# Kernel tuning notes

Measured on AMD Instinct MI355X. Metric: run time of the kernel, lower is better.

## Reference

```python
import jax, jax.numpy as jnp
import numpy as np

N_NODES = 50000


def setup_inputs() -> dict:
    key = jax.random.key(0)
    k = jax.random.split(key, 5)
    x = jax.random.normal(k[0], (N_NODES, 64), dtype=jnp.float32)
    edge_index = jax.random.randint(k[1], (2, 800000), 0, N_NODES, dtype=jnp.int64)
    # Glorot-ish init for weights
    W1 = jax.random.normal(k[2], (64, 64), dtype=jnp.float32) * (1.0 / np.sqrt(64))
    b1 = jnp.zeros((64,), dtype=jnp.float32)
    W2 = jax.random.normal(k[3], (64, 16), dtype=jnp.float32) * (1.0 / np.sqrt(64))
    b2 = jnp.zeros((16,), dtype=jnp.float32)
    return {"x": x, "edge_index": edge_index, "W1": W1, "b1": b1, "W2": W2, "b2": b2}


def _gcn_conv(h, row, col, W, b, n_nodes):
    # PyG GCNConv: add self-loops, symmetric deg normalization, linear, scatter-add.
    h = h @ W                                   # [N, out]
    deg = jax.ops.segment_sum(jnp.ones_like(col, dtype=h.dtype), col,
                              num_segments=n_nodes)          # in-degree incl. self-loops
    dinv = jnp.where(deg > 0, jax.lax.rsqrt(deg), 0.0)       # deg^{-1/2}
    norm = dinv[row] * dinv[col]                             # [E]
    msg = h[row] * norm[:, None]                             # gather + scale, [E, out]
    out = jax.ops.segment_sum(msg, col, num_segments=n_nodes)  # scatter-add at targets
    return out + b


def reference(x, edge_index, W1, b1, W2, b2):
    n = x.shape[0]
    loops = jnp.arange(n, dtype=edge_index.dtype)
    row = jnp.concatenate([edge_index[0], loops])  # sources (with self-loops)
    col = jnp.concatenate([edge_index[1], loops])  # targets (with self-loops)
    h = _gcn_conv(x, row, col, W1, b1, n)
    h = jax.nn.relu(h)
    h = _gcn_conv(h, row, col, W2, b2, n)
    return jax.nn.log_softmax(h, axis=1)
```

## Files before the change

### kernel.cpp

```cpp
#include <hip/hip_runtime.h>
#include <hip/hip_bf16.h>
#include <math.h>


#define BLK 256
#define EPB 2048
#define GSH 9
#define GMASK 511
#define GMAX 128
#define QCAP 10240

typedef __attribute__((ext_vector_type(8))) short short8;
typedef __attribute__((ext_vector_type(4))) float float4v;
typedef __attribute__((ext_vector_type(4))) unsigned short ushort4v;

__device__ __forceinline__ short f2bf(float f) {
    __hip_bfloat16 h = __float2bfloat16(f);
    union { __hip_bfloat16 h; short s; } u; u.h = h; return u.s;
}
__device__ __forceinline__ float bf2f(short s) {
    union { short s; __hip_bfloat16 h; } u; u.s = s; return __bfloat162float(u.h);
}
__device__ __forceinline__ float ldf(const void* p, long long i, int f32) {
    if (f32) return ((const float*)p)[i];
    return __bfloat162float(((const __hip_bfloat16*)p)[i]);
}
__device__ __forceinline__ float4v mfma_bf16(short8 a, short8 b, float4v c) {
    return __builtin_amdgcn_mfma_f32_16x16x32_bf16(a, b, c, 0, 0, 0);
}

__global__ void init_k(const void* edge_raw, const unsigned short* xraw, long long n_nodes,
                       const void* W1, const void* W2, const void* b1, const void* b2,
                       int* flags, short* wT1, short* wT2, float* b1f, float* b2f,
                       int* gtail, int G) {
    __shared__ int bad, cnt;
    int tid = threadIdx.x;
    if (tid == 0) { bad = 0; cnt = 0; }
    __syncthreads();
    const long long* p = (const long long*)edge_raw;
    for (int i = tid; i < 1024; i += BLK) {
        long long v = p[i];
        if (v < 0 || v >= n_nodes) bad = 1;
    }
    int e = (xraw[2 * tid] >> 7) & 0xFF;
    int inr = (e >= 96 && e <= 130) ? 1 : 0;
    __syncthreads();
    if (inr) atomicAdd(&cnt, 1);
    __syncthreads();
    int f32 = (cnt < 128) ? 1 : 0;
    if (tid == 0) { flags[0] = bad ? 0 : 1; flags[1] = f32; }
    for (int i = tid; i < G * 16; i += BLK) gtail[i] = 0;
    for (int idx = tid; idx < 4096; idx += BLK) {
        int k = idx >> 6, j = idx & 63;
        wT1[j * 64 + k] = f2bf(ldf(W1, idx, f32));
    }
    for (int idx = tid; idx < 1024; idx += BLK) {
        int k = idx >> 4, j = idx & 15;
        wT2[j * 64 + k] = f2bf(ldf(W2, idx, f32));
    }
    if (tid < 64) b1f[tid] = ldf(b1, tid, f32);
    if (tid < 16) b2f[tid] = ldf(b2, tid, f32);
}

__global__ __launch_bounds__(BLK) void binAmm1_k(const void* edge_raw, const void* x,
                                                 const int* __restrict__ flags, int E,
                                                 int* gtail, int* __restrict__ queue,
                                                 const short* __restrict__ wT1,
                                                 unsigned short* __restrict__ h1,
                                                 int N, int G, int nblkA) {
    int bid = blockIdx.x, tid = threadIdx.x;
    if (bid < nblkA) {
        __shared__ int hist[GMAX], base[GMAX];
        for (int g = tid; g < G; g += BLK) hist[g] = 0;
        __syncthreads();
        int is64 = flags[0];
        int e0 = bid * EPB;
        int r[8], c[8], pos[8];
        const long long* p64 = (const long long*)edge_raw;
        const int* p32 = (const int*)edge_raw;
        #pragma unroll
        for (int i = 0; i < 8; ++i) {
            int e = e0 + i * BLK + tid;
            int rr = -1, cc = 0;
            if (e < E) {
                if (is64) { rr = (int)p64[e]; cc = (int)p64[(long long)E + e]; }
                else      { rr = p32[e];      cc = p32[E + e]; }
            }
            r[i] = rr; c[i] = cc;
            pos[i] = (rr >= 0) ? atomicAdd(&hist[cc >> GSH], 1) : 0;
        }
        __syncthreads();
        for (int g = tid; g < G; g += BLK) {
            int h = hist[g];
            base[g] = h ? atomicAdd(&gtail[g << 4], h) : 0;
        }
        __syncthreads();
        #pragma unroll
        for (int i = 0; i < 8; ++i) {
            if (r[i] >= 0) {
                int g = c[i] >> GSH;
                int idx = base[g] + pos[i];
                if (idx < QCAP)
                    queue[(long long)g * QCAP + idx] = (r[i] << GSH) | (c[i] & GMASK);
            }
        }
    } else {
        int wave = ((bid - nblkA) << 2) + (tid >> 6);
        int lane = tid & 63;
        int node0 = wave << 4;
        if (node0 >= N) return;
        int m = lane & 15, quad = lane >> 4;
        int node = node0 + m;
        int nc = node < N ? node : N - 1;
        short8 a0, a1;
        if (flags[1]) {
            const float* xf = (const float*)x + ((long long)nc << 6) + quad * 8;
            #pragma unroll
            for (int i = 0; i < 8; ++i) { a0[i] = f2bf(xf[i]); a1[i] = f2bf(xf[32 + i]); }
        } else {
            const unsigned short* xb = (const unsigned short*)x + ((long long)nc << 6) + quad * 8;
            a0 = *(const short8*)xb;
            a1 = *(const short8*)(xb + 32);
        }
        const short8* wp = (const short8*)wT1;
        #pragma unroll
        for (int jt = 0; jt < 4; ++jt) {
            float4v cc = {0.f, 0.f, 0.f, 0.f};
            cc = mfma_bf16(a0, wp[((jt * 16 + m) << 3) + quad], cc);
            cc = mfma_bf16(a1, wp[((jt * 16 + m) << 3) + 4 + quad], cc);
            #pragma unroll
            for (int r2 = 0; r2 < 4; ++r2) {
                int n2 = node0 + (quad << 2) + r2;
                if (n2 < N) h1[((long long)n2 << 6) + jt * 16 + m] = (unsigned short)f2bf(cc[r2]);
            }
        }
    }
}

__global__ __launch_bounds__(1024) void binB_k(const int* __restrict__ gtail,
                                               const int* __restrict__ queue,
                                               unsigned short* __restrict__ srcs,
                                               int* __restrict__ cntf,
                                               float* __restrict__ dinv, int N) {
    __shared__ int lcnt[512];
    int g = blockIdx.x, tid = threadIdx.x;
    for (int i = tid; i < 512; i += 1024) lcnt[i] = 0;
    __syncthreads();
    int len = gtail[g << 4];
    if (len > QCAP) len = QCAP;
    const int* q = queue + (long long)g * QCAP;
    int n0 = g << GSH;
    for (int i = tid; i < len; i += 1024) {
        int u = q[i];
        int cl = u & GMASK, rr = u >> GSH;
        int pos = atomicAdd(&lcnt[cl], 1);
        if (pos < 64) srcs[((long long)(n0 + cl) << 6) + pos] = (unsigned short)rr;
    }
    __syncthreads();
    for (int i = tid; i < 512; i += 1024) {
        int gn = n0 + i;
        if (gn < N) {
            cntf[gn] = lcnt[i];
            dinv[gn] = rsqrtf((float)lcnt[i] + 1.0f);
        }
    }
}

__global__ __launch_bounds__(BLK) void agg1mm2_k(const unsigned short* __restrict__ h1,
                                                 const int* __restrict__ cntf,
                                                 const float* __restrict__ dinv,
                                                 const unsigned short* __restrict__ srcs,
                                                 const short* __restrict__ wT2,
                                                 const float* __restrict__ b1f,
                                                 unsigned short* __restrict__ h2, int N) {
    __shared__ short a_lds[16][72];
    int b = blockIdx.x, tid = threadIdx.x;
    int wv = tid >> 6, lane = tid & 63;
    int seg = lane & 7;
    int es  = lane >> 3;
    #pragma unroll
    for (int k = 0; k < 4; ++k) {
        int nl = wv * 4 + k;
        int gn = (b << 4) + nl;
        int gnc = gn < N ? gn : N - 1;
        float acc[8];
        #pragma unroll
        for (int i = 0; i < 8; ++i) acc[i] = 0.f;
        float dc = 1.f;
        if (gn < N) {
            int dg = cntf[gn];
            int m = dg < 64 ? dg : 64;
            const unsigned short* sp = srcs + ((long long)gn << 6);
            dc = dinv[gn];
            for (int e = es; e < m; e += 8) {
                int r = sp[e];
                float d = dinv[r];
                short8 v = *(const short8*)(h1 + ((long long)r << 6) + (seg << 3));
                #pragma unroll
                for (int i = 0; i < 8; ++i) acc[i] += bf2f(v[i]) * d;
            }
        }
        #pragma unroll
        for (int i = 0; i < 8; ++i) {
            acc[i] += __shfl_xor(acc[i], 8, 64);
            acc[i] += __shfl_xor(acc[i], 16, 64);
            acc[i] += __shfl_xor(acc[i], 32, 64);
        }
        if (es == 0) {
            short8 vs = *(const short8*)(h1 + ((long long)gnc << 6) + (seg << 3));
            short8 o;
            #pragma unroll
            for (int i = 0; i < 8; ++i) {
                float hg = (gn < N) ? (acc[i] + bf2f(vs[i]) * dc) * dc : 0.f;
                o[i] = f2bf(fmaxf(hg + b1f[(seg << 3) + i], 0.f));
            }
            *(short8*)&a_lds[nl][seg << 3] = o;
        }
    }
    __syncthreads();
    if (wv == 0) {
        int m = lane & 15, quad = lane >> 4;
        short8 a0 = *(const short8*)&a_lds[m][quad * 8];
        short8 a1 = *(const short8*)&a_lds[m][quad * 8 + 32];
        const short8* wp = (const short8*)wT2;
        float4v c = {0.f, 0.f, 0.f, 0.f};
        c = mfma_bf16(a0, wp[(m << 3) + quad], c);
        c = mfma_bf16(a1, wp[(m << 3) + 4 + quad], c);
        #pragma unroll
        for (int r = 0; r < 4; ++r) {
            int n2 = (b << 4) + (quad << 2) + r;
            if (n2 < N) h2[((long long)n2 << 4) + m] = (unsigned short)f2bf(c[r] * dinv[n2]);
        }
    }
}

__global__ __launch_bounds__(BLK) void agg2sm_k(const unsigned short* __restrict__ h2,
                                                const int* __restrict__ cntf,
                                                const unsigned short* __restrict__ srcs,
                                                const float* __restrict__ b2f,
                                                const int* __restrict__ flags,
                                                void* __restrict__ out, int N) {
    int c = (blockIdx.x * BLK + threadIdx.x) >> 6;
    if (c >= N) return;
    int lane = threadIdx.x & 63;
    int seg = lane & 1;
    int es  = lane >> 1;
    int dg = cntf[c];
    int m = dg < 64 ? dg : 64;
    const unsigned short* sp = srcs + ((long long)c << 6);
    float acc[8];
    #pragma unroll
    for (int i = 0; i < 8; ++i) acc[i] = 0.f;
    for (int e = es; e < m; e += 32) {
        int r = sp[e];
        short8 v = *(const short8*)(h2 + ((long long)r << 4) + (seg << 3));
        #pragma unroll
        for (int i = 0; i < 8; ++i) acc[i] += bf2f(v[i]);
    }
    #pragma unroll
    for (int i = 0; i < 8; ++i) {
        acc[i] += __shfl_xor(acc[i], 2, 64);
        acc[i] += __shfl_xor(acc[i], 4, 64);
        acc[i] += __shfl_xor(acc[i], 8, 64);
        acc[i] += __shfl_xor(acc[i], 16, 64);
        acc[i] += __shfl_xor(acc[i], 32, 64);
    }
    float dc = rsqrtf((float)dg + 1.0f);
    short8 vs = *(const short8*)(h2 + ((long long)c << 4) + (seg << 3));
    float logit[8];
    float mx = -1e30f;
    #pragma unroll
    for (int i = 0; i < 8; ++i) {
        logit[i] = (acc[i] + bf2f(vs[i])) * dc + b2f[(seg << 3) + i];
        mx = fmaxf(mx, logit[i]);
    }
    mx = fmaxf(mx, __shfl_xor(mx, 1, 64));
    float s = 0.f;
    #pragma unroll
    for (int i = 0; i < 8; ++i) s += expf(logit[i] - mx);
    s += __shfl_xor(s, 1, 64);
    float lse = mx + logf(s);
    if (es == 0) {
        if (flags[1]) {
            float* op = (float*)out + ((long long)c << 4) + (seg << 3);
            #pragma unroll
            for (int i = 0; i < 8; ++i) op[i] = logit[i] - lse;
        } else {
            __hip_bfloat16* op = (__hip_bfloat16*)out + ((long long)c << 4) + (seg << 3);
            #pragma unroll
            for (int i = 0; i < 8; ++i) op[i] = __float2bfloat16(logit[i] - lse);
        }
    }
}

extern "C" void kernel_launch(void* const* d_in, const int* in_sizes, int n_in,
                              void* d_out, int out_size, void* d_ws, size_t ws_size,
                              hipStream_t stream) {
    const void* x        = d_in[0];
    const void* edge_raw = d_in[1];
    const void* W1       = d_in[2];
    const void* b1       = d_in[3];
    const void* W2       = d_in[4];
    const void* b2       = d_in[5];

    const int N = in_sizes[0] / 64;
    const int E = in_sizes[1] / 2;
    const int G = (N + 511) >> 9;
    const int NBUCK = (N + 15) / 16;

    char* ws = (char*)d_ws;
    size_t o = 0;
    auto take = [&](size_t bytes) { char* p = ws + o; o += (bytes + 255) & ~(size_t)255; return p; };
    int*            flags  = (int*)take(256);
    int*            gtail  = (int*)take((size_t)G * 64);
    int*            queue  = (int*)take((size_t)G * QCAP * 4);
    unsigned short* srcs   = (unsigned short*)take((size_t)N * 64 * 2);
    int*            cntf   = (int*)take((size_t)N * 4);
    float*          dinv   = (float*)take((size_t)N * 4);
    float*          b1f    = (float*)take(64 * 4);
    float*          b2f    = (float*)take(16 * 4);
    short*          wT1    = (short*)take(4096 * 2);
    short*          wT2    = (short*)take(1024 * 2);
    unsigned short* h1     = (unsigned short*)take((size_t)N * 64 * 2);
    unsigned short* h2     = (unsigned short*)take((size_t)N * 16 * 2);

    int nblkA = (E + EPB - 1) / EPB;
    int nblkW = ((N + 15) / 16 + 3) / 4;
    int nblkG = ((size_t)N * 64 + BLK - 1) / BLK;

    init_k<<<1, BLK, 0, stream>>>(edge_raw, (const unsigned short*)x, (long long)N,
                                  W1, W2, b1, b2, flags, wT1, wT2, b1f, b2f, gtail, G);
    binAmm1_k<<<nblkA + nblkW, BLK, 0, stream>>>(edge_raw, x, flags, E, gtail, queue,
                                                 wT1, h1, N, G, nblkA);
    binB_k<<<G, 1024, 0, stream>>>(gtail, queue, srcs, cntf, dinv, N);
    agg1mm2_k<<<NBUCK, BLK, 0, stream>>>(h1, cntf, dinv, srcs, wT2, b1f, h2, N);
    agg2sm_k<<<nblkG, BLK, 0, stream>>>(h2, cntf, srcs, b2f, flags, d_out, N);
}
```

Measured before the change: 161.7 us.

## Aggregate directly from bucketed edge queues with LDS float atomics, drop CSR build

Buckets shrink to 128 target nodes. The per-node source list (srcs/cntf) is no longer built; a lightweight degree kernel counts in-degrees from the queue. Both aggregation kernels now run one block per bucket, stream that bucket's edge queue and scatter-add gathered features into a shared-memory accumulator with LDS atomics, then apply normalization, MM2 and log-softmax. This removes the 64-neighbor cap and one intermediate write/read pass, at the cost of many LDS float atomics, fewer and larger blocks, and a fixed QCAP of 3072 per bucket that could overflow on skewed graphs.

```diff
diff --git a/kernel.cpp b/kernel.cpp
--- a/kernel.cpp
+++ b/kernel.cpp
@@ -4,15 +4,14 @@
 
 
 #define BLK 256
-#define EPB 2048
-#define GSH 9
-#define GMASK 511
-#define GMAX 128
-#define QCAP 10240
+#define EPB 4096
+#define GSH 7
+#define GMASK 127
+#define GMAX 512
+#define QCAP 3072
 
 typedef __attribute__((ext_vector_type(8))) short short8;
 typedef __attribute__((ext_vector_type(4))) float float4v;
-typedef __attribute__((ext_vector_type(4))) unsigned short ushort4v;
 
 __device__ __forceinline__ short f2bf(float f) {
     __hip_bfloat16 h = __float2bfloat16(f);
@@ -75,11 +74,11 @@
         __syncthreads();
         int is64 = flags[0];
         int e0 = bid * EPB;
-        int r[8], c[8], pos[8];
+        int r[16], c[16], pos[16];
         const long long* p64 = (const long long*)edge_raw;
         const int* p32 = (const int*)edge_raw;
         #pragma unroll
-        for (int i = 0; i < 8; ++i) {
+        for (int i = 0; i < 16; ++i) {
             int e = e0 + i * BLK + tid;
             int rr = -1, cc = 0;
             if (e < E) {
@@ -96,7 +95,7 @@
         }
         __syncthreads();
         #pragma unroll
-        for (int i = 0; i < 8; ++i) {
+        for (int i = 0; i < 16; ++i) {
             if (r[i] >= 0) {
                 int g = c[i] >> GSH;
                 int idx = base[g] + pos[i];
@@ -137,158 +136,143 @@
     }
 }
 
-__global__ __launch_bounds__(1024) void binB_k(const int* __restrict__ gtail,
-                                               const int* __restrict__ queue,
-                                               unsigned short* __restrict__ srcs,
-                                               int* __restrict__ cntf,
-                                               float* __restrict__ dinv, int N) {
-    __shared__ int lcnt[512];
+__global__ __launch_bounds__(BLK) void deg_k(const int* __restrict__ gtail,
+                                             const int* __restrict__ queue,
+                                             float* __restrict__ dinv, int N) {
+    __shared__ int cnt[128];
     int g = blockIdx.x, tid = threadIdx.x;
-    for (int i = tid; i < 512; i += 1024) lcnt[i] = 0;
+    if (tid < 128) cnt[tid] = 0;
     __syncthreads();
     int len = gtail[g << 4];
     if (len > QCAP) len = QCAP;
     const int* q = queue + (long long)g * QCAP;
-    int n0 = g << GSH;
-    for (int i = tid; i < len; i += 1024) {
-        int u = q[i];
-        int cl = u & GMASK, rr = u >> GSH;
-        int pos = atomicAdd(&lcnt[cl], 1);
-        if (pos < 64) srcs[((long long)(n0 + cl) << 6) + pos] = (unsigned short)rr;
-    }
-    __syncthreads();
-    for (int i = tid; i < 512; i += 1024) {
-        int gn = n0 + i;
-        if (gn < N) {
-            cntf[gn] = lcnt[i];
-            dinv[gn] = rsqrtf((float)lcnt[i] + 1.0f);
-        }
-    }
-}
-
-__global__ __launch_bounds__(BLK) void agg1mm2_k(const unsigned short* __restrict__ h1,
-                                                 const int* __restrict__ cntf,
+    for (int i = tid; i < len; i += BLK)
+        atomicAdd(&cnt[q[i] & GMASK], 1);
+    __syncthreads();
+    if (tid < 128) {
+        int gn = (g << GSH) + tid;
+        if (gn < N) dinv[gn] = rsqrtf((float)cnt[tid] + 1.0f);
+    }
+}
+
+__global__ __launch_bounds__(512) void agg1mm2_k(const unsigned short* __restrict__ h1,
                                                  const float* __restrict__ dinv,
-                                                 const unsigned short* __restrict__ srcs,
+                                                 const int* __restrict__ gtail,
+                                                 const int* __restrict__ queue,
                                                  const short* __restrict__ wT2,
                                                  const float* __restrict__ b1f,
                                                  unsigned short* __restrict__ h2, int N) {
-    __shared__ short a_lds[16][72];
-    int b = blockIdx.x, tid = threadIdx.x;
+    __shared__ float acc[128][67];
+    int g = blockIdx.x, tid = threadIdx.x;
+    float* af = &acc[0][0];
+    for (int i = tid; i < 128 * 67; i += 512) af[i] = 0.f;
+    __syncthreads();
+    int len = gtail[g << 4];
+    if (len > QCAP) len = QCAP;
+    const int* q = queue + (long long)g * QCAP;
     int wv = tid >> 6, lane = tid & 63;
-    int seg = lane & 7;
-    int es  = lane >> 3;
-    #pragma unroll
-    for (int k = 0; k < 4; ++k) {
-        int nl = wv * 4 + k;
-        int gn = (b << 4) + nl;
-        int gnc = gn < N ? gn : N - 1;
-        float acc[8];
-        #pragma unroll
-        for (int i = 0; i < 8; ++i) acc[i] = 0.f;
-        float dc = 1.f;
-        if (gn < N) {
-            int dg = cntf[gn];
-            int m = dg < 64 ? dg : 64;
-            const unsigned short* sp = srcs + ((long long)gn << 6);
-            dc = dinv[gn];
-            for (int e = es; e < m; e += 8) {
-                int r = sp[e];
-                float d = dinv[r];
-                short8 v = *(const short8*)(h1 + ((long long)r << 6) + (seg << 3));
-                #pragma unroll
-                for (int i = 0; i < 8; ++i) acc[i] += bf2f(v[i]) * d;
-            }
-        }
+    int es = lane >> 3, seg = lane & 7;
+    for (int e0 = wv * 8; e0 < len; e0 += 64) {
+        int e = e0 + es;
+        if (e < len) {
+            int u = q[e];
+            int r = u >> GSH, cl = u & GMASK;
+            float d = dinv[r];
+            short8 v = *(const short8*)(h1 + ((long long)r << 6) + (seg << 3));
+            #pragma unroll
+            for (int i = 0; i < 8; ++i)
+                atomicAdd(&acc[cl][(seg << 3) + i], bf2f(v[i]) * d);
+        }
+    }
+    __syncthreads();
+    {
+        int m = lane & 15, quad = lane >> 4;
+        int node = (wv << 4) + m;
+        int gn = (g << GSH) + node;
+        int gc = gn < N ? gn : N - 1;
+        float dc = dinv[gc];
+        const unsigned short* hs = h1 + ((long long)gc << 6);
+        short8 s0 = *(const short8*)(hs + quad * 8);
+        short8 s1 = *(const short8*)(hs + quad * 8 + 32);
+        short8 a0, a1;
         #pragma unroll
         for (int i = 0; i < 8; ++i) {
-            acc[i] += __shfl_xor(acc[i], 8, 64);
-            acc[i] += __shfl_xor(acc[i], 16, 64);
-            acc[i] += __shfl_xor(acc[i], 32, 64);
-        }
-        if (es == 0) {
-            short8 vs = *(const short8*)(h1 + ((long long)gnc << 6) + (seg << 3));
-            short8 o;
-            #pragma unroll
-            for (int i = 0; i < 8; ++i) {
-                float hg = (gn < N) ? (acc[i] + bf2f(vs[i]) * dc) * dc : 0.f;
-                o[i] = f2bf(fmaxf(hg + b1f[(seg << 3) + i], 0.f));
-            }
-            *(short8*)&a_lds[nl][seg << 3] = o;
-        }
-    }
-    __syncthreads();
-    if (wv == 0) {
-        int m = lane & 15, quad = lane >> 4;
-        short8 a0 = *(const short8*)&a_lds[m][quad * 8];
-        short8 a1 = *(const short8*)&a_lds[m][quad * 8 + 32];
+            int f0 = quad * 8 + i, f1 = f0 + 32;
+            float v0 = (acc[node][f0] + bf2f(s0[i]) * dc) * dc + b1f[f0];
+            float v1 = (acc[node][f1] + bf2f(s1[i]) * dc) * dc + b1f[f1];
+            a0[i] = f2bf(fmaxf(v0, 0.f));
+            a1[i] = f2bf(fmaxf(v1, 0.f));
+        }
         const short8* wp = (const short8*)wT2;
         float4v c = {0.f, 0.f, 0.f, 0.f};
         c = mfma_bf16(a0, wp[(m << 3) + quad], c);
         c = mfma_bf16(a1, wp[(m << 3) + 4 + quad], c);
         #pragma unroll
-        for (int r = 0; r < 4; ++r) {
-            int n2 = (b << 4) + (quad << 2) + r;
-            if (n2 < N) h2[((long long)n2 << 4) + m] = (unsigned short)f2bf(c[r] * dinv[n2]);
+        for (int r2 = 0; r2 < 4; ++r2) {
+            int n2 = (g << GSH) + (wv << 4) + (quad << 2) + r2;
+            if (n2 < N) h2[((long long)n2 << 4) + m] = (unsigned short)f2bf(c[r2] * dinv[n2]);
         }
     }
 }
 
 __global__ __launch_bounds__(BLK) void agg2sm_k(const unsigned short* __restrict__ h2,
-                                                const int* __restrict__ cntf,
-                                                const unsigned short* __restrict__ srcs,
+                                                const float* __restrict__ dinv,
+                                                const int* __restrict__ gtail,
+                                                const int* __restrict__ queue,
                                                 const float* __restrict__ b2f,
                                                 const int* __restrict__ flags,
                                                 void* __restrict__ out, int N) {
-    int c = (blockIdx.x * BLK + threadIdx.x) >> 6;
-    if (c >= N) return;
-    int lane = threadIdx.x & 63;
-    int seg = lane & 1;
-    int es  = lane >> 1;
-    int dg = cntf[c];
-    int m = dg < 64 ? dg : 64;
-    const unsigned short* sp = srcs + ((long long)c << 6);
-    float acc[8];
-    #pragma unroll
-    for (int i = 0; i < 8; ++i) acc[i] = 0.f;
-    for (int e = es; e < m; e += 32) {
-        int r = sp[e];
-        short8 v = *(const short8*)(h2 + ((long long)r << 4) + (seg << 3));
-        #pragma unroll
-        for (int i = 0; i < 8; ++i) acc[i] += bf2f(v[i]);
-    }
-    #pragma unroll
-    for (int i = 0; i < 8; ++i) {
-        acc[i] += __shfl_xor(acc[i], 2, 64);
-        acc[i] += __shfl_xor(acc[i], 4, 64);
-        acc[i] += __shfl_xor(acc[i], 8, 64);
-        acc[i] += __shfl_xor(acc[i], 16, 64);
-        acc[i] += __shfl_xor(acc[i], 32, 64);
-    }
-    float dc = rsqrtf((float)dg + 1.0f);
-    short8 vs = *(const short8*)(h2 + ((long long)c << 4) + (seg << 3));
-    float logit[8];
-    float mx = -1e30f;
-    #pragma unroll
-    for (int i = 0; i < 8; ++i) {
-        logit[i] = (acc[i] + bf2f(vs[i])) * dc + b2f[(seg << 3) + i];
-        mx = fmaxf(mx, logit[i]);
-    }
-    mx = fmaxf(mx, __shfl_xor(mx, 1, 64));
-    float s = 0.f;
-    #pragma unroll
-    for (int i = 0; i < 8; ++i) s += expf(logit[i] - mx);
-    s += __shfl_xor(s, 1, 64);
-    float lse = mx + logf(s);
-    if (es == 0) {
-        if (flags[1]) {
-            float* op = (float*)out + ((long long)c << 4) + (seg << 3);
-            #pragma unroll
-            for (int i = 0; i < 8; ++i) op[i] = logit[i] - lse;
-        } else {
-            __hip_bfloat16* op = (__hip_bfloat16*)out + ((long long)c << 4) + (seg << 3);
-            #pragma unroll
-            for (int i = 0; i < 8; ++i) op[i] = __float2bfloat16(logit[i] - lse);
+    __shared__ float acc[128][21];
+    int g = blockIdx.x, tid = threadIdx.x;
+    float* af = &acc[0][0];
+    for (int i = tid; i < 128 * 21; i += BLK) af[i] = 0.f;
+    __syncthreads();
+    int len = gtail[g << 4];
+    if (len > QCAP) len = QCAP;
+    const int* q = queue + (long long)g * QCAP;
+    int wv = tid >> 6, lane = tid & 63;
+    int es = lane >> 1, sg = lane & 1;
+    for (int e0 = wv * 32; e0 < len; e0 += 128) {
+        int e = e0 + es;
+        if (e < len) {
+            int u = q[e];
+            int r = u >> GSH, cl = u & GMASK;
+            short8 v = *(const short8*)(h2 + ((long long)r << 4) + (sg << 3));
+            #pragma unroll
+            for (int i = 0; i < 8; ++i)
+                atomicAdd(&acc[cl][(sg << 3) + i], bf2f(v[i]));
+        }
+    }
+    __syncthreads();
+    if (tid < 128) {
+        int gn = (g << GSH) + tid;
+        if (gn < N) {
+            float dc = dinv[gn];
+            const unsigned short* hs = h2 + ((long long)gn << 4);
+            short8 v0 = *(const short8*)hs;
+            short8 v1 = *(const short8*)(hs + 8);
+            float lg[16];
+            float mx = -1e30f;
+            #pragma unroll
+            for (int j = 0; j < 8; ++j) {
+                lg[j]     = (acc[tid][j]     + bf2f(v0[j])) * dc + b2f[j];
+                lg[j + 8] = (acc[tid][j + 8] + bf2f(v1[j])) * dc + b2f[j + 8];
+            }
+            #pragma unroll
+            for (int j = 0; j < 16; ++j) mx = fmaxf(mx, lg[j]);
+            float s = 0.f;
+            #pragma unroll
+            for (int j = 0; j < 16; ++j) s += expf(lg[j] - mx);
+            float lse = mx + logf(s);
+            if (flags[1]) {
+                float* op = (float*)out + ((long long)gn << 4);
+                #pragma unroll
+                for (int j = 0; j < 16; ++j) op[j] = lg[j] - lse;
+            } else {
+                __hip_bfloat16* op = (__hip_bfloat16*)out + ((long long)gn << 4);
+                #pragma unroll
+                for (int j = 0; j < 16; ++j) op[j] = __float2bfloat16(lg[j] - lse);
+            }
         }
     }
 }
@@ -305,8 +289,7 @@
 
     const int N = in_sizes[0] / 64;
     const int E = in_sizes[1] / 2;
-    const int G = (N + 511) >> 9;
-    const int NBUCK = (N + 15) / 16;
+    const int G = (N + GMASK) >> GSH;
 
     char* ws = (char*)d_ws;
     size_t o = 0;
@@ -314,8 +297,6 @@
     int*            flags  = (int*)take(256);
     int*            gtail  = (int*)take((size_t)G * 64);
     int*            queue  = (int*)take((size_t)G * QCAP * 4);
-    unsigned short* srcs   = (unsigned short*)take((size_t)N * 64 * 2);
-    int*            cntf   = (int*)take((size_t)N * 4);
     float*          dinv   = (float*)take((size_t)N * 4);
     float*          b1f    = (float*)take(64 * 4);
     float*          b2f    = (float*)take(16 * 4);
@@ -326,13 +307,12 @@
 
     int nblkA = (E + EPB - 1) / EPB;
     int nblkW = ((N + 15) / 16 + 3) / 4;
-    int nblkG = ((size_t)N * 64 + BLK - 1) / BLK;
 
     init_k<<<1, BLK, 0, stream>>>(edge_raw, (const unsigned short*)x, (long long)N,
                                   W1, W2, b1, b2, flags, wT1, wT2, b1f, b2f, gtail, G);
     binAmm1_k<<<nblkA + nblkW, BLK, 0, stream>>>(edge_raw, x, flags, E, gtail, queue,
                                                  wT1, h1, N, G, nblkA);
-    binB_k<<<G, 1024, 0, stream>>>(gtail, queue, srcs, cntf, dinv, N);
-    agg1mm2_k<<<NBUCK, BLK, 0, stream>>>(h1, cntf, dinv, srcs, wT2, b1f, h2, N);
-    agg2sm_k<<<nblkG, BLK, 0, stream>>>(h2, cntf, srcs, b2f, flags, d_out, N);
-}
+    deg_k<<<G, BLK, 0, stream>>>(gtail, queue, dinv, N);
+    agg1mm2_k<<<G, 512, 0, stream>>>(h1, dinv, gtail, queue, wT2, b1f, h2, N);
+    agg2sm_k<<<G, BLK, 0, stream>>>(h2, dinv, gtail, queue, b2f, flags, d_out, N);
+}
```

New measurement: 546.0 us. +237.8%, slower.

## Replace two-pass bucketed edge binning with direct global-atomic CSR fill

Applied to the files above, without the earlier changes.

Drops the two-stage binning (block histograms into per-group queues, then a separate per-group kernel building per-node source lists) and instead has each edge atomically increment a global per-node counter and write its source straight into that node's slot list. This removes one kernel launch, the queue buffer and its round trip through memory, and the dinv array, which is now recomputed with rsqrt from the counts where needed. In exchange it relies on heavy global atomics to random addresses. It also adds extra count loads in the aggregation kernel for every neighbour.

```diff
diff --git a/kernel.cpp b/kernel.cpp
--- a/kernel.cpp
+++ b/kernel.cpp
@@ -4,15 +4,10 @@
 
 
 #define BLK 256
-#define EPB 2048
-#define GSH 9
-#define GMASK 511
-#define GMAX 128
-#define QCAP 10240
+#define EPB 1024
 
 typedef __attribute__((ext_vector_type(8))) short short8;
 typedef __attribute__((ext_vector_type(4))) float float4v;
-typedef __attribute__((ext_vector_type(4))) unsigned short ushort4v;
 
 __device__ __forceinline__ short f2bf(float f) {
     __hip_bfloat16 h = __float2bfloat16(f);
@@ -32,10 +27,12 @@
 __global__ void init_k(const void* edge_raw, const unsigned short* xraw, long long n_nodes,
                        const void* W1, const void* W2, const void* b1, const void* b2,
                        int* flags, short* wT1, short* wT2, float* b1f, float* b2f,
-                       int* gtail, int G) {
-    __shared__ int bad, cnt;
-    int tid = threadIdx.x;
-    if (tid == 0) { bad = 0; cnt = 0; }
+                       int* cnt, int N) {
+    int tid = threadIdx.x, bid = blockIdx.x;
+    for (int i = bid * BLK + tid; i < N; i += gridDim.x * BLK) cnt[i] = 0;
+    if (bid != 0) return;
+    __shared__ int bad, scnt;
+    if (tid == 0) { bad = 0; scnt = 0; }
     __syncthreads();
     const long long* p = (const long long*)edge_raw;
     for (int i = tid; i < 1024; i += BLK) {
@@ -45,11 +42,10 @@
     int e = (xraw[2 * tid] >> 7) & 0xFF;
     int inr = (e >= 96 && e <= 130) ? 1 : 0;
     __syncthreads();
-    if (inr) atomicAdd(&cnt, 1);
-    __syncthreads();
-    int f32 = (cnt < 128) ? 1 : 0;
+    if (inr) atomicAdd(&scnt, 1);
+    __syncthreads();
+    int f32 = (scnt < 128) ? 1 : 0;
     if (tid == 0) { flags[0] = bad ? 0 : 1; flags[1] = f32; }
-    for (int i = tid; i < G * 16; i += BLK) gtail[i] = 0;
     for (int idx = tid; idx < 4096; idx += BLK) {
         int k = idx >> 6, j = idx & 63;
         wT1[j * 64 + k] = f2bf(ldf(W1, idx, f32));
@@ -64,44 +60,29 @@
 
 __global__ __launch_bounds__(BLK) void binAmm1_k(const void* edge_raw, const void* x,
                                                  const int* __restrict__ flags, int E,
-                                                 int* gtail, int* __restrict__ queue,
+                                                 int* __restrict__ cnt,
+                                                 unsigned short* __restrict__ srcs,
                                                  const short* __restrict__ wT1,
                                                  unsigned short* __restrict__ h1,
-                                                 int N, int G, int nblkA) {
+                                                 int N, int nblkA) {
     int bid = blockIdx.x, tid = threadIdx.x;
     if (bid < nblkA) {
-        __shared__ int hist[GMAX], base[GMAX];
-        for (int g = tid; g < G; g += BLK) hist[g] = 0;
-        __syncthreads();
         int is64 = flags[0];
-        int e0 = bid * EPB;
-        int r[8], c[8], pos[8];
         const long long* p64 = (const long long*)edge_raw;
         const int* p32 = (const int*)edge_raw;
-        #pragma unroll
-        for (int i = 0; i < 8; ++i) {
+        int e0 = bid * EPB;
+        #pragma unroll
+        for (int i = 0; i < EPB / BLK; ++i) {
             int e = e0 + i * BLK + tid;
-            int rr = -1, cc = 0;
             if (e < E) {
+                int rr, cc;
                 if (is64) { rr = (int)p64[e]; cc = (int)p64[(long long)E + e]; }
                 else      { rr = p32[e];      cc = p32[E + e]; }
-            }
-            r[i] = rr; c[i] = cc;
-            pos[i] = (rr >= 0) ? atomicAdd(&hist[cc >> GSH], 1) : 0;
-        }
-        __syncthreads();
-        for (int g = tid; g < G; g += BLK) {
-            int h = hist[g];
-            base[g] = h ? atomicAdd(&gtail[g << 4], h) : 0;
-        }
-        __syncthreads();
-        #pragma unroll
-        for (int i = 0; i < 8; ++i) {
-            if (r[i] >= 0) {
-                int g = c[i] >> GSH;
-                int idx = base[g] + pos[i];
-                if (idx < QCAP)
-                    queue[(long long)g * QCAP + idx] = (r[i] << GSH) | (c[i] & GMASK);
+                if ((unsigned)rr < (unsigned)N && (unsigned)cc < (unsigned)N) {
+                    int pos = atomicAdd(&cnt[cc], 1);
+                    if (pos < 64)
+                        srcs[((long long)cc << 6) + pos] = (unsigned short)rr;
+                }
             }
         }
     } else {
@@ -137,38 +118,8 @@
     }
 }
 
-__global__ __launch_bounds__(1024) void binB_k(const int* __restrict__ gtail,
-                                               const int* __restrict__ queue,
-                                               unsigned short* __restrict__ srcs,
-                                               int* __restrict__ cntf,
-                                               float* __restrict__ dinv, int N) {
-    __shared__ int lcnt[512];
-    int g = blockIdx.x, tid = threadIdx.x;
-    for (int i = tid; i < 512; i += 1024) lcnt[i] = 0;
-    __syncthreads();
-    int len = gtail[g << 4];
-    if (len > QCAP) len = QCAP;
-    const int* q = queue + (long long)g * QCAP;
-    int n0 = g << GSH;
-    for (int i = tid; i < len; i += 1024) {
-        int u = q[i];
-        int cl = u & GMASK, rr = u >> GSH;
-        int pos = atomicAdd(&lcnt[cl], 1);
-        if (pos < 64) srcs[((long long)(n0 + cl) << 6) + pos] = (unsigned short)rr;
-    }
-    __syncthreads();
-    for (int i = tid; i < 512; i += 1024) {
-        int gn = n0 + i;
-        if (gn < N) {
-            cntf[gn] = lcnt[i];
-            dinv[gn] = rsqrtf((float)lcnt[i] + 1.0f);
-        }
-    }
-}
-
 __global__ __launch_bounds__(BLK) void agg1mm2_k(const unsigned short* __restrict__ h1,
-                                                 const int* __restrict__ cntf,
-                                                 const float* __restrict__ dinv,
+                                                 const int* __restrict__ cnt,
                                                  const unsigned short* __restrict__ srcs,
                                                  const short* __restrict__ wT2,
                                                  const float* __restrict__ b1f,
@@ -188,13 +139,13 @@
         for (int i = 0; i < 8; ++i) acc[i] = 0.f;
         float dc = 1.f;
         if (gn < N) {
-            int dg = cntf[gn];
+            int dg = cnt[gn];
             int m = dg < 64 ? dg : 64;
             const unsigned short* sp = srcs + ((long long)gn << 6);
-            dc = dinv[gn];
+            dc = rsqrtf((float)dg + 1.0f);
             for (int e = es; e < m; e += 8) {
                 int r = sp[e];
-                float d = dinv[r];
+                float d = rsqrtf((float)cnt[r] + 1.0f);
                 short8 v = *(const short8*)(h1 + ((long long)r << 6) + (seg << 3));
                 #pragma unroll
                 for (int i = 0; i < 8; ++i) acc[i] += bf2f(v[i]) * d;
@@ -229,13 +180,16 @@
         #pragma unroll
         for (int r = 0; r < 4; ++r) {
             int n2 = (b << 4) + (quad << 2) + r;
-            if (n2 < N) h2[((long long)n2 << 4) + m] = (unsigned short)f2bf(c[r] * dinv[n2]);
+            if (n2 < N) {
+                float dv = rsqrtf((float)cnt[n2] + 1.0f);
+                h2[((long long)n2 << 4) + m] = (unsigned short)f2bf(c[r] * dv);
+            }
         }
     }
 }
 
 __global__ __launch_bounds__(BLK) void agg2sm_k(const unsigned short* __restrict__ h2,
-                                                const int* __restrict__ cntf,
+                                                const int* __restrict__ cnt,
                                                 const unsigned short* __restrict__ srcs,
                                                 const float* __restrict__ b2f,
                                                 const int* __restrict__ flags,
@@ -245,7 +199,7 @@
     int lane = threadIdx.x & 63;
     int seg = lane & 1;
     int es  = lane >> 1;
-    int dg = cntf[c];
+    int dg = cnt[c];
     int m = dg < 64 ? dg : 64;
     const unsigned short* sp = srcs + ((long long)c << 6);
     float acc[8];
@@ -305,18 +259,13 @@
 
     const int N = in_sizes[0] / 64;
     const int E = in_sizes[1] / 2;
-    const int G = (N + 511) >> 9;
-    const int NBUCK = (N + 15) / 16;
 
     char* ws = (char*)d_ws;
     size_t o = 0;
     auto take = [&](size_t bytes) { char* p = ws + o; o += (bytes + 255) & ~(size_t)255; return p; };
     int*            flags  = (int*)take(256);
-    int*            gtail  = (int*)take((size_t)G * 64);
-    int*            queue  = (int*)take((size_t)G * QCAP * 4);
+    int*            cnt    = (int*)take((size_t)N * 4);
     unsigned short* srcs   = (unsigned short*)take((size_t)N * 64 * 2);
-    int*            cntf   = (int*)take((size_t)N * 4);
-    float*          dinv   = (float*)take((size_t)N * 4);
     float*          b1f    = (float*)take(64 * 4);
     float*          b2f    = (float*)take(16 * 4);
     short*          wT1    = (short*)take(4096 * 2);
@@ -326,13 +275,13 @@
 
     int nblkA = (E + EPB - 1) / EPB;
     int nblkW = ((N + 15) / 16 + 3) / 4;
+    int NBUCK = (N + 15) / 16;
     int nblkG = ((size_t)N * 64 + BLK - 1) / BLK;
 
-    init_k<<<1, BLK, 0, stream>>>(edge_raw, (const unsigned short*)x, (long long)N,
-                                  W1, W2, b1, b2, flags, wT1, wT2, b1f, b2f, gtail, G);
-    binAmm1_k<<<nblkA + nblkW, BLK, 0, stream>>>(edge_raw, x, flags, E, gtail, queue,
-                                                 wT1, h1, N, G, nblkA);
-    binB_k<<<G, 1024, 0, stream>>>(gtail, queue, srcs, cntf, dinv, N);
-    agg1mm2_k<<<NBUCK, BLK, 0, stream>>>(h1, cntf, dinv, srcs, wT2, b1f, h2, N);
-    agg2sm_k<<<nblkG, BLK, 0, stream>>>(h2, cntf, srcs, b2f, flags, d_out, N);
-}
+    init_k<<<64, BLK, 0, stream>>>(edge_raw, (const unsigned short*)x, (long long)N,
+                                   W1, W2, b1, b2, flags, wT1, wT2, b1f, b2f, cnt, N);
+    binAmm1_k<<<nblkA + nblkW, BLK, 0, stream>>>(edge_raw, x, flags, E, cnt, srcs,
+                                                 wT1, h1, N, nblkA);
+    agg1mm2_k<<<NBUCK, BLK, 0, stream>>>(h1, cnt, srcs, wT2, b1f, h2, N);
+    agg2sm_k<<<nblkG, BLK, 0, stream>>>(h2, cnt, srcs, b2f, flags, d_out, N);
+}
```

Result: slower. 197.1 us (+21.9%).
